# Kernel optimization log

Measured on AMD Instinct MI355X. Metric: run time of the kernel, lower is better.

The kernel has to match this reference:

```python
import jax, jax.numpy as jnp
import numpy as np

# Static hyperparameters (match init_kwargs)
VAR_WEIGHT = 1.0
DIST_WEIGHT = 1.0
MARGIN_VAR = 0.5
MARGIN_DIST = 3.0
IGNORE_LABEL = 255
C = 8  # max instance id present in generated gt (labels 1..8; 0 = background)


def setup_inputs() -> dict:
    key = jax.random.key(0)
    k1, k2 = jax.random.split(key)
    featmap = jax.random.normal(k1, (16, 1, 720, 1280), dtype=jnp.float32)
    gt = jax.random.randint(k2, (16, 1, 720, 1280), 0, 9, dtype=jnp.int64)
    return {"featmap": featmap, "gt": gt}


def reference(featmap, gt):
    B = featmap.shape[0]
    x = featmap.reshape(B, -1)                      # [B, N]
    g = gt.reshape(B, -1)
    # labels >= ignore_label contribute nothing; map them to background (0),
    # which is already excluded (instance ids start at 1).
    g = jnp.where(g < IGNORE_LABEL, g, 0).astype(jnp.int32)

    # segment id = batch * (C+1) + label  -> per-(batch, instance) reductions
    nseg = B * (C + 1)
    seg = (jnp.arange(B, dtype=jnp.int32)[:, None] * (C + 1) + g).reshape(-1)
    xf = x.reshape(-1)

    cnt = jax.ops.segment_sum(jnp.ones_like(xf), seg, num_segments=nseg)
    ssum = jax.ops.segment_sum(xf, seg, num_segments=nseg)
    mean = ssum / jnp.maximum(cnt, 1.0)             # per-instance mean

    # pull: per-element hinge on |x - mean_i|, then per-instance mean
    pe = jnp.maximum(jnp.abs(xf - mean[seg]) - MARGIN_VAR, 0.0) ** 2
    psum = jax.ops.segment_sum(pe, seg, num_segments=nseg)
    pull_inst = (psum / jnp.maximum(cnt, 1.0)).reshape(B, C + 1)[:, 1:]   # [B, C]
    valid = (cnt > 0).reshape(B, C + 1)[:, 1:]                             # [B, C]
    vf = valid.astype(xf.dtype)
    n_pull = vf.sum()
    fallback = 0.0 * featmap.mean()
    pull_loss = jnp.where(
        n_pull > 0, (pull_inst * vf).sum() / jnp.maximum(n_pull, 1.0), fallback
    ) * VAR_WEIGHT

    # push: all ordered pairs i != j of present instances within each batch
    means = mean.reshape(B, C + 1)[:, 1:]                                  # [B, C]
    d = jnp.abs(means[:, :, None] - means[:, None, :])                     # [B, C, C]
    pair = vf[:, :, None] * vf[:, None, :] * (1.0 - jnp.eye(C, dtype=xf.dtype))
    ploss = jnp.maximum(2.0 * MARGIN_DIST - d, 0.0) ** 2
    n_push = pair.sum()
    push_loss = jnp.where(
        n_push > 0, (ploss * pair).sum() / jnp.maximum(n_push, 1.0), fallback
    ) * DIST_WEIGHT

    return push_loss + pull_loss
```

## Files before the change

kernel.cpp:

```cpp
#include <hip/hip_runtime.h>

#define BATCH 16
#define NINST 8
#define NPB   (720 * 1280)
#define NV4   (NPB / 4)
#define BLKX  225
#define MARGIN_VAR  0.5f
#define MARGIN_DIST 3.0f


__device__ __forceinline__ void acc_stats(float4 xv, int4 gv,
                                          float (&s)[NINST], float (&c)[NINST]) {
#pragma unroll
    for (int l = 1; l <= NINST; ++l) {
        bool m0 = (gv.x == l), m1 = (gv.y == l), m2 = (gv.z == l), m3 = (gv.w == l);
        s[l - 1] += (m0 ? xv.x : 0.f) + (m1 ? xv.y : 0.f)
                  + (m2 ? xv.z : 0.f) + (m3 ? xv.w : 0.f);
        c[l - 1] += (m0 ? 1.f : 0.f) + (m1 ? 1.f : 0.f)
                  + (m2 ? 1.f : 0.f) + (m3 ? 1.f : 0.f);
    }
}

__global__ __launch_bounds__(256) void k_stats(const float4* __restrict__ x,
                                               const int4* __restrict__ g,
                                               float* __restrict__ ws) {
    const int b = blockIdx.y;
    const size_t base = (size_t)b * NV4 + (size_t)blockIdx.x * 1024 + threadIdx.x;

    float4 xv0 = x[base];
    float4 xv1 = x[base + 256];
    float4 xv2 = x[base + 512];
    float4 xv3 = x[base + 768];
    int4   gv0 = g[base];
    int4   gv1 = g[base + 256];
    int4   gv2 = g[base + 512];
    int4   gv3 = g[base + 768];

    float s[NINST], c[NINST];
#pragma unroll
    for (int l = 0; l < NINST; ++l) { s[l] = 0.f; c[l] = 0.f; }

    acc_stats(xv0, gv0, s, c);
    acc_stats(xv1, gv1, s, c);
    acc_stats(xv2, gv2, s, c);
    acc_stats(xv3, gv3, s, c);

#pragma unroll
    for (int l = 0; l < NINST; ++l) {
#pragma unroll
        for (int off = 32; off; off >>= 1) {
            s[l] += __shfl_down(s[l], off);
            c[l] += __shfl_down(c[l], off);
        }
    }

    __shared__ float red[4][2 * NINST];
    const int lane = threadIdx.x & 63, wid = threadIdx.x >> 6;
    if (lane == 0) {
#pragma unroll
        for (int l = 0; l < NINST; ++l) {
            red[wid][l]         = c[l];
            red[wid][NINST + l] = s[l];
        }
    }
    __syncthreads();
    if (threadIdx.x < 2 * NINST) {
        float v = red[0][threadIdx.x] + red[1][threadIdx.x] +
                  red[2][threadIdx.x] + red[3][threadIdx.x];
        int l     = threadIdx.x & (NINST - 1);
        int isSum = threadIdx.x >> 3;
        atomicAdd(&ws[isSum * 128 + b * NINST + l], v);
    }
}

__device__ __forceinline__ void acc_pull(float4 xv, int4 gv,
                                         const float* __restrict__ smu,
                                         float (&p)[NINST]) {
    int g0 = ((unsigned)gv.x <= NINST) ? gv.x : 0;
    int g1 = ((unsigned)gv.y <= NINST) ? gv.y : 0;
    int g2 = ((unsigned)gv.z <= NINST) ? gv.z : 0;
    int g3 = ((unsigned)gv.w <= NINST) ? gv.w : 0;
    float t0 = fmaxf(fabsf(xv.x - smu[g0]) - MARGIN_VAR, 0.f);
    float t1 = fmaxf(fabsf(xv.y - smu[g1]) - MARGIN_VAR, 0.f);
    float t2 = fmaxf(fabsf(xv.z - smu[g2]) - MARGIN_VAR, 0.f);
    float t3 = fmaxf(fabsf(xv.w - smu[g3]) - MARGIN_VAR, 0.f);
    float p0 = t0 * t0, p1 = t1 * t1, p2 = t2 * t2, p3 = t3 * t3;
#pragma unroll
    for (int l = 1; l <= NINST; ++l) {
        p[l - 1] += ((g0 == l) ? p0 : 0.f) + ((g1 == l) ? p1 : 0.f)
                  + ((g2 == l) ? p2 : 0.f) + ((g3 == l) ? p3 : 0.f);
    }
}

__global__ __launch_bounds__(256) void k_pull(const float4* __restrict__ x,
                                              const int4* __restrict__ g,
                                              float* __restrict__ ws) {
    const int b = blockIdx.y;
    const size_t base = (size_t)b * NV4 + (size_t)blockIdx.x * 1024 + threadIdx.x;

    float4 xv0 = x[base];
    float4 xv1 = x[base + 256];
    float4 xv2 = x[base + 512];
    float4 xv3 = x[base + 768];
    int4   gv0 = g[base];
    int4   gv1 = g[base + 256];
    int4   gv2 = g[base + 512];
    int4   gv3 = g[base + 768];

    __shared__ float smu[NINST + 1];
    if (threadIdx.x == 0) smu[0] = 0.f;
    if (threadIdx.x < NINST) {
        float cnt = ws[b * NINST + threadIdx.x];
        float sum = ws[128 + b * NINST + threadIdx.x];
        smu[1 + threadIdx.x] = sum / fmaxf(cnt, 1.f);
    }
    __syncthreads();

    float p[NINST];
#pragma unroll
    for (int l = 0; l < NINST; ++l) p[l] = 0.f;

    acc_pull(xv0, gv0, smu, p);
    acc_pull(xv1, gv1, smu, p);
    acc_pull(xv2, gv2, smu, p);
    acc_pull(xv3, gv3, smu, p);

#pragma unroll
    for (int l = 0; l < NINST; ++l) {
#pragma unroll
        for (int off = 32; off; off >>= 1)
            p[l] += __shfl_down(p[l], off);
    }

    __shared__ float red[4][NINST];
    const int lane = threadIdx.x & 63, wid = threadIdx.x >> 6;
    if (lane == 0) {
#pragma unroll
        for (int l = 0; l < NINST; ++l) red[wid][l] = p[l];
    }
    __syncthreads();
    if (threadIdx.x < NINST) {
        float v = red[0][threadIdx.x] + red[1][threadIdx.x] +
                  red[2][threadIdx.x] + red[3][threadIdx.x];
        atomicAdd(&ws[256 + b * NINST + threadIdx.x], v);
    }
}

__global__ __launch_bounds__(128) void k_final(const float* __restrict__ ws,
                                               float* __restrict__ out) {
    const int tid = threadIdx.x;
    const int b = tid >> 3;

    float cnt = ws[tid];
    float sum = ws[128 + tid];
    float ps  = ws[256 + tid];
    float valid  = (cnt > 0.f) ? 1.f : 0.f;
    float mean   = sum / fmaxf(cnt, 1.f);
    float pull_i = ps / fmaxf(cnt, 1.f);

    __shared__ float smean[128];
    __shared__ float svalid[128];
    smean[tid]  = mean;
    svalid[tid] = valid;
    __syncthreads();

    float ploss = 0.f, npush = 0.f;
#pragma unroll
    for (int j = 0; j < NINST; ++j) {
        if (j == (tid & 7)) continue;
        float pv = valid * svalid[b * NINST + j];
        float d  = fabsf(mean - smean[b * NINST + j]);
        float t  = fmaxf(2.f * MARGIN_DIST - d, 0.f);
        ploss += pv * t * t;
        npush += pv;
    }

    float vals[4] = {pull_i * valid, valid, ploss, npush};
#pragma unroll
    for (int k = 0; k < 4; ++k) {
#pragma unroll
        for (int off = 32; off; off >>= 1)
            vals[k] += __shfl_down(vals[k], off);
    }

    __shared__ float r2[2][4];
    const int lane = tid & 63, wid = tid >> 6;
    if (lane == 0) {
#pragma unroll
        for (int k = 0; k < 4; ++k) r2[wid][k] = vals[k];
    }
    __syncthreads();
    if (tid == 0) {
        float pulls = r2[0][0] + r2[1][0];
        float npl   = r2[0][1] + r2[1][1];
        float pls   = r2[0][2] + r2[1][2];
        float nps   = r2[0][3] + r2[1][3];
        float pull_loss = (npl > 0.f) ? pulls / fmaxf(npl, 1.f) : 0.f;
        float push_loss = (nps > 0.f) ? pls / fmaxf(nps, 1.f) : 0.f;
        out[0] = push_loss + pull_loss;
    }
}

extern "C" void kernel_launch(void* const* d_in, const int* in_sizes, int n_in,
                              void* d_out, int out_size, void* d_ws, size_t ws_size,
                              hipStream_t stream) {
    const float* x = (const float*)d_in[0];
    const int*   g = (const int*)d_in[1];
    float* out = (float*)d_out;
    float* ws  = (float*)d_ws;

    hipMemsetAsync(d_ws, 0, 384 * sizeof(float), stream);

    dim3 grid(BLKX, BATCH);
    k_stats<<<grid, 256, 0, stream>>>((const float4*)x, (const int4*)g, ws);
    k_pull<<<grid, 256, 0, stream>>>((const float4*)x, (const int4*)g, ws);
    k_final<<<1, 128, 0, stream>>>(ws, out);
}
```

Baseline: 164.9 us.

## Precompute per-instance weights so pull pass accumulates one scalar; ballot-based counts

A small middle kernel computes per-instance means, the push loss, and a combined pull weight valid/(cnt*n_pull), stored as (mean, weight) pairs with a zero entry for background. The pull pass then does one table lookup and one FMA per element into a single accumulator, replacing eight per-label select-accumulates and eight shuffle reductions. The stats pass counts with wave ballot and popcount instead of float select-adds. This adds an extra kernel launch, and ballot per label per element may cost more than the float adds it replaces.

```diff
diff --git a/kernel.cpp b/kernel.cpp
--- a/kernel.cpp
+++ b/kernel.cpp
@@ -10,22 +10,27 @@
 
 
 __device__ __forceinline__ void acc_stats(float4 xv, int4 gv,
-                                          float (&s)[NINST], float (&c)[NINST]) {
-#pragma unroll
-    for (int l = 1; l <= NINST; ++l) {
-        bool m0 = (gv.x == l), m1 = (gv.y == l), m2 = (gv.z == l), m3 = (gv.w == l);
-        s[l - 1] += (m0 ? xv.x : 0.f) + (m1 ? xv.y : 0.f)
-                  + (m2 ? xv.z : 0.f) + (m3 ? xv.w : 0.f);
-        c[l - 1] += (m0 ? 1.f : 0.f) + (m1 ? 1.f : 0.f)
-                  + (m2 ? 1.f : 0.f) + (m3 ? 1.f : 0.f);
+                                          float (&s)[NINST], int (&cw)[NINST]) {
+#pragma unroll
+    for (int e = 0; e < 4; ++e) {
+        int   li = (e == 0) ? gv.x : (e == 1) ? gv.y : (e == 2) ? gv.z : gv.w;
+        float xx = (e == 0) ? xv.x : (e == 1) ? xv.y : (e == 2) ? xv.z : xv.w;
+        int l = ((unsigned)li <= NINST) ? li : 0;
+#pragma unroll
+        for (int q = 1; q <= NINST; ++q) {
+            bool eq = (l == q);
+            s[q - 1] += eq ? xx : 0.f;
+            cw[q - 1] += (int)__popcll(__ballot(eq));
+        }
     }
 }
 
 __global__ __launch_bounds__(256) void k_stats(const float4* __restrict__ x,
                                                const int4* __restrict__ g,
                                                float* __restrict__ ws) {
+    const int tid = threadIdx.x;
     const int b = blockIdx.y;
-    const size_t base = (size_t)b * NV4 + (size_t)blockIdx.x * 1024 + threadIdx.x;
+    const size_t base = (size_t)b * NV4 + (size_t)blockIdx.x * 1024 + tid;
 
     float4 xv0 = x[base];
     float4 xv1 = x[base + 256];
@@ -36,67 +41,119 @@
     int4   gv2 = g[base + 512];
     int4   gv3 = g[base + 768];
 
-    float s[NINST], c[NINST];
-#pragma unroll
-    for (int l = 0; l < NINST; ++l) { s[l] = 0.f; c[l] = 0.f; }
-
-    acc_stats(xv0, gv0, s, c);
-    acc_stats(xv1, gv1, s, c);
-    acc_stats(xv2, gv2, s, c);
-    acc_stats(xv3, gv3, s, c);
+    float s[NINST];
+    int   cw[NINST];
+#pragma unroll
+    for (int l = 0; l < NINST; ++l) { s[l] = 0.f; cw[l] = 0; }
+
+    acc_stats(xv0, gv0, s, cw);
+    acc_stats(xv1, gv1, s, cw);
+    acc_stats(xv2, gv2, s, cw);
+    acc_stats(xv3, gv3, s, cw);
 
 #pragma unroll
     for (int l = 0; l < NINST; ++l) {
 #pragma unroll
-        for (int off = 32; off; off >>= 1) {
+        for (int off = 32; off; off >>= 1)
             s[l] += __shfl_down(s[l], off);
-            c[l] += __shfl_down(c[l], off);
-        }
     }
 
     __shared__ float red[4][2 * NINST];
-    const int lane = threadIdx.x & 63, wid = threadIdx.x >> 6;
+    const int lane = tid & 63, wid = tid >> 6;
     if (lane == 0) {
 #pragma unroll
         for (int l = 0; l < NINST; ++l) {
-            red[wid][l]         = c[l];
+            red[wid][l]         = (float)cw[l];
             red[wid][NINST + l] = s[l];
         }
     }
     __syncthreads();
-    if (threadIdx.x < 2 * NINST) {
-        float v = red[0][threadIdx.x] + red[1][threadIdx.x] +
-                  red[2][threadIdx.x] + red[3][threadIdx.x];
-        int l     = threadIdx.x & (NINST - 1);
-        int isSum = threadIdx.x >> 3;
+    if (tid < 2 * NINST) {
+        float v = red[0][tid] + red[1][tid] + red[2][tid] + red[3][tid];
+        int l     = tid & (NINST - 1);
+        int isSum = tid >> 3;
         atomicAdd(&ws[isSum * 128 + b * NINST + l], v);
     }
 }
 
+__global__ __launch_bounds__(128) void k_mid(float* __restrict__ ws) {
+    const int tid = threadIdx.x;
+    const int b = tid >> 3;
+
+    float cnt = ws[tid];
+    float sum = ws[128 + tid];
+    float valid = (cnt > 0.f) ? 1.f : 0.f;
+    float mean  = sum / fmaxf(cnt, 1.f);
+
+    __shared__ float smean[128];
+    __shared__ float svalid[128];
+    smean[tid]  = mean;
+    svalid[tid] = valid;
+    __syncthreads();
+
+    float ploss = 0.f, npush = 0.f;
+#pragma unroll
+    for (int j = 0; j < NINST; ++j) {
+        if (j == (tid & 7)) continue;
+        float pv = valid * svalid[b * NINST + j];
+        float d  = fabsf(mean - smean[b * NINST + j]);
+        float t  = fmaxf(2.f * MARGIN_DIST - d, 0.f);
+        ploss += pv * t * t;
+        npush += pv;
+    }
+
+    float vals[3] = {valid, ploss, npush};
+#pragma unroll
+    for (int k = 0; k < 3; ++k) {
+#pragma unroll
+        for (int off = 32; off; off >>= 1)
+            vals[k] += __shfl_down(vals[k], off);
+    }
+
+    __shared__ float r2[2][3];
+    __shared__ float snp;
+    const int lane = tid & 63, wid = tid >> 6;
+    if (lane == 0) {
+#pragma unroll
+        for (int k = 0; k < 3; ++k) r2[wid][k] = vals[k];
+    }
+    __syncthreads();
+    if (tid == 0) {
+        float npl = r2[0][0] + r2[1][0];
+        float pls = r2[0][1] + r2[1][1];
+        float nps = r2[0][2] + r2[1][2];
+        ws[440] = (nps > 0.f) ? pls / fmaxf(nps, 1.f) : 0.f;
+        snp = npl;
+    }
+    __syncthreads();
+
+    float n_pull = snp;
+    float w = (n_pull > 0.f) ? valid / (fmaxf(cnt, 1.f) * n_pull) : 0.f;
+    float2* mw = (float2*)(ws + 448);
+    mw[b * 9 + (tid & 7) + 1] = make_float2(mean, w);
+    if (tid < BATCH) mw[tid * 9] = make_float2(0.f, 0.f);
+}
+
 __device__ __forceinline__ void acc_pull(float4 xv, int4 gv,
-                                         const float* __restrict__ smu,
-                                         float (&p)[NINST]) {
-    int g0 = ((unsigned)gv.x <= NINST) ? gv.x : 0;
-    int g1 = ((unsigned)gv.y <= NINST) ? gv.y : 0;
-    int g2 = ((unsigned)gv.z <= NINST) ? gv.z : 0;
-    int g3 = ((unsigned)gv.w <= NINST) ? gv.w : 0;
-    float t0 = fmaxf(fabsf(xv.x - smu[g0]) - MARGIN_VAR, 0.f);
-    float t1 = fmaxf(fabsf(xv.y - smu[g1]) - MARGIN_VAR, 0.f);
-    float t2 = fmaxf(fabsf(xv.z - smu[g2]) - MARGIN_VAR, 0.f);
-    float t3 = fmaxf(fabsf(xv.w - smu[g3]) - MARGIN_VAR, 0.f);
-    float p0 = t0 * t0, p1 = t1 * t1, p2 = t2 * t2, p3 = t3 * t3;
-#pragma unroll
-    for (int l = 1; l <= NINST; ++l) {
-        p[l - 1] += ((g0 == l) ? p0 : 0.f) + ((g1 == l) ? p1 : 0.f)
-                  + ((g2 == l) ? p2 : 0.f) + ((g3 == l) ? p3 : 0.f);
-    }
-}
-
-__global__ __launch_bounds__(256) void k_pull(const float4* __restrict__ x,
-                                              const int4* __restrict__ g,
-                                              float* __restrict__ ws) {
+                                         const float2* __restrict__ smw,
+                                         float& acc) {
+#pragma unroll
+    for (int e = 0; e < 4; ++e) {
+        int   li = (e == 0) ? gv.x : (e == 1) ? gv.y : (e == 2) ? gv.z : gv.w;
+        float xx = (e == 0) ? xv.x : (e == 1) ? xv.y : (e == 2) ? xv.z : xv.w;
+        int l = ((unsigned)li <= NINST) ? li : 0;
+        float2 mw = smw[l];
+        float t = fmaxf(fabsf(xx - mw.x) - MARGIN_VAR, 0.f);
+        acc = fmaf(t * t, mw.y, acc);
+    }
+}
+
+__global__ __launch_bounds__(256) void k_pull2(const float4* __restrict__ x,
+                                               const int4* __restrict__ g,
+                                               float* __restrict__ ws) {
+    const int tid = threadIdx.x;
     const int b = blockIdx.y;
-    const size_t base = (size_t)b * NV4 + (size_t)blockIdx.x * 1024 + threadIdx.x;
+    const size_t base = (size_t)b * NV4 + (size_t)blockIdx.x * 1024 + tid;
 
     float4 xv0 = x[base];
     float4 xv1 = x[base + 256];
@@ -107,112 +164,53 @@
     int4   gv2 = g[base + 512];
     int4   gv3 = g[base + 768];
 
-    __shared__ float smu[NINST + 1];
-    if (threadIdx.x == 0) smu[0] = 0.f;
-    if (threadIdx.x < NINST) {
-        float cnt = ws[b * NINST + threadIdx.x];
-        float sum = ws[128 + b * NINST + threadIdx.x];
-        smu[1 + threadIdx.x] = sum / fmaxf(cnt, 1.f);
-    }
-    __syncthreads();
-
-    float p[NINST];
-#pragma unroll
-    for (int l = 0; l < NINST; ++l) p[l] = 0.f;
-
-    acc_pull(xv0, gv0, smu, p);
-    acc_pull(xv1, gv1, smu, p);
-    acc_pull(xv2, gv2, smu, p);
-    acc_pull(xv3, gv3, smu, p);
-
-#pragma unroll
-    for (int l = 0; l < NINST; ++l) {
-#pragma unroll
-        for (int off = 32; off; off >>= 1)
-            p[l] += __shfl_down(p[l], off);
-    }
-
-    __shared__ float red[4][NINST];
-    const int lane = threadIdx.x & 63, wid = threadIdx.x >> 6;
-    if (lane == 0) {
-#pragma unroll
-        for (int l = 0; l < NINST; ++l) red[wid][l] = p[l];
-    }
-    __syncthreads();
-    if (threadIdx.x < NINST) {
-        float v = red[0][threadIdx.x] + red[1][threadIdx.x] +
-                  red[2][threadIdx.x] + red[3][threadIdx.x];
-        atomicAdd(&ws[256 + b * NINST + threadIdx.x], v);
-    }
-}
-
-__global__ __launch_bounds__(128) void k_final(const float* __restrict__ ws,
+    __shared__ float2 smw[16];
+    if (tid < 9) smw[tid] = ((const float2*)(ws + 448))[b * 9 + tid];
+    __syncthreads();
+
+    float acc = 0.f;
+    acc_pull(xv0, gv0, smw, acc);
+    acc_pull(xv1, gv1, smw, acc);
+    acc_pull(xv2, gv2, smw, acc);
+    acc_pull(xv3, gv3, smw, acc);
+
+#pragma unroll
+    for (int off = 32; off; off >>= 1)
+        acc += __shfl_down(acc, off);
+
+    __shared__ float red[4];
+    const int lane = tid & 63, wid = tid >> 6;
+    if (lane == 0) red[wid] = acc;
+    __syncthreads();
+    if (tid == 0) {
+        float v = red[0] + red[1] + red[2] + red[3];
+        atomicAdd(&ws[400 + b], v);
+    }
+}
+
+__global__ __launch_bounds__(64) void k_final2(const float* __restrict__ ws,
                                                float* __restrict__ out) {
     const int tid = threadIdx.x;
-    const int b = tid >> 3;
-
-    float cnt = ws[tid];
-    float sum = ws[128 + tid];
-    float ps  = ws[256 + tid];
-    float valid  = (cnt > 0.f) ? 1.f : 0.f;
-    float mean   = sum / fmaxf(cnt, 1.f);
-    float pull_i = ps / fmaxf(cnt, 1.f);
-
-    __shared__ float smean[128];
-    __shared__ float svalid[128];
-    smean[tid]  = mean;
-    svalid[tid] = valid;
-    __syncthreads();
-
-    float ploss = 0.f, npush = 0.f;
-#pragma unroll
-    for (int j = 0; j < NINST; ++j) {
-        if (j == (tid & 7)) continue;
-        float pv = valid * svalid[b * NINST + j];
-        float d  = fabsf(mean - smean[b * NINST + j]);
-        float t  = fmaxf(2.f * MARGIN_DIST - d, 0.f);
-        ploss += pv * t * t;
-        npush += pv;
-    }
-
-    float vals[4] = {pull_i * valid, valid, ploss, npush};
-#pragma unroll
-    for (int k = 0; k < 4; ++k) {
-#pragma unroll
-        for (int off = 32; off; off >>= 1)
-            vals[k] += __shfl_down(vals[k], off);
-    }
-
-    __shared__ float r2[2][4];
-    const int lane = tid & 63, wid = tid >> 6;
-    if (lane == 0) {
-#pragma unroll
-        for (int k = 0; k < 4; ++k) r2[wid][k] = vals[k];
-    }
-    __syncthreads();
-    if (tid == 0) {
-        float pulls = r2[0][0] + r2[1][0];
-        float npl   = r2[0][1] + r2[1][1];
-        float pls   = r2[0][2] + r2[1][2];
-        float nps   = r2[0][3] + r2[1][3];
-        float pull_loss = (npl > 0.f) ? pulls / fmaxf(npl, 1.f) : 0.f;
-        float push_loss = (nps > 0.f) ? pls / fmaxf(nps, 1.f) : 0.f;
-        out[0] = push_loss + pull_loss;
-    }
+    float v = (tid < BATCH) ? ws[400 + tid] : 0.f;
+#pragma unroll
+    for (int off = 8; off; off >>= 1)
+        v += __shfl_down(v, off);
+    if (tid == 0) out[0] = ws[440] + v;
 }
 
 extern "C" void kernel_launch(void* const* d_in, const int* in_sizes, int n_in,
                               void* d_out, int out_size, void* d_ws, size_t ws_size,
                               hipStream_t stream) {
-    const float* x = (const float*)d_in[0];
-    const int*   g = (const int*)d_in[1];
+    const float4* x4 = (const float4*)d_in[0];
+    const int4*   g4 = (const int4*)d_in[1];
     float* out = (float*)d_out;
     float* ws  = (float*)d_ws;
 
-    hipMemsetAsync(d_ws, 0, 384 * sizeof(float), stream);
+    hipMemsetAsync(d_ws, 0, 3072, stream);
 
     dim3 grid(BLKX, BATCH);
-    k_stats<<<grid, 256, 0, stream>>>((const float4*)x, (const int4*)g, ws);
-    k_pull<<<grid, 256, 0, stream>>>((const float4*)x, (const int4*)g, ws);
-    k_final<<<1, 128, 0, stream>>>(ws, out);
-}
+    k_stats<<<grid, 256, 0, stream>>>(x4, g4, ws);
+    k_mid<<<1, 128, 0, stream>>>(ws);
+    k_pull2<<<grid, 256, 0, stream>>>(x4, g4, ws);
+    k_final2<<<1, 64, 0, stream>>>(ws, out);
+}
```

Measured after the change: 195.7 us. +18.6%, slower.
